# Performance work log

Hardware: AMD Instinct MI355X
Metric: run time of the kernel (lower is better)

Reference implementation:

```python
import jax, jax.numpy as jnp
import numpy as np

EMBED_DIM = 1024
N_HEADS = 16
HEAD_DIM = EMBED_DIM // N_HEADS


def setup_inputs() -> dict:
    key = jax.random.key(0)
    k_x, k_qw, k_qb, k_ow, k_ob = jax.random.split(key, 5)
    s = 1.0 / np.sqrt(EMBED_DIM)
    return {
        "x": jax.random.normal(k_x, (2, 2048, EMBED_DIM), dtype=jnp.float32),
        "qkv_w": jax.random.uniform(k_qw, (3 * EMBED_DIM, EMBED_DIM), jnp.float32, -s, s),
        "qkv_b": jax.random.uniform(k_qb, (3 * EMBED_DIM,), jnp.float32, -s, s),
        "out_w": jax.random.uniform(k_ow, (EMBED_DIM, EMBED_DIM), jnp.float32, -s, s),
        "out_b": jax.random.uniform(k_ob, (EMBED_DIM,), jnp.float32, -s, s),
    }


def reference(x, qkv_w, qkv_b, out_w, out_b):
    B, S, E = x.shape
    # fused QKV projection (torch Linear: x @ W^T + b)
    qkv = x @ qkv_w.T + qkv_b                      # [B,S,3E]
    qkv = qkv.reshape(B, S, N_HEADS, 3 * HEAD_DIM).transpose(0, 2, 1, 3)  # [B,H,S,3d]
    q, k, v = jnp.split(qkv, 3, axis=-1)           # each [B,H,S,d]
    scores = jnp.einsum("bhqd,bhkd->bhqk", q, k) / jnp.sqrt(jnp.float32(HEAD_DIM))
    weights = jax.nn.softmax(scores, axis=-1)      # [B,H,S,S]
    attn = jnp.einsum("bhqk,bhkd->bhqd", weights, v)
    attn = attn.transpose(0, 2, 1, 3).reshape(B, S, E)
    return attn @ out_w.T + out_b
```

## Files before the change

### kernel.cpp

```cpp
#include <hip/hip_runtime.h>
#include <hip/hip_bf16.h>


#define E_DIM   1024
#define NHEADS  16
#define HDIM    64
#define SEQ     2048
#define TOK     4096
#define QKV_DIM 3072
#define QK_STRIDE 2048
#define QSCALE_F 0.18033688011112042f

typedef __attribute__((ext_vector_type(8))) short bf16x8;
typedef __attribute__((ext_vector_type(4))) float f32x4;
typedef __attribute__((ext_vector_type(4))) int   i32x4;
typedef __attribute__((ext_vector_type(2))) int   i32x2;
typedef __attribute__((ext_vector_type(2))) __bf16 bf16x2_t;

#if __has_builtin(__builtin_amdgcn_exp2f)
#define EXP2F(x) __builtin_amdgcn_exp2f(x)
#else
#define EXP2F(x) exp2f(x)
#endif

__device__ __forceinline__ unsigned pack2bf(float a, float b) {
#if __has_builtin(__builtin_amdgcn_cvt_pk_bf16_f32)
    union { bf16x2_t v; unsigned u; } u;
    u.v = __builtin_amdgcn_cvt_pk_bf16_f32(a, b);
    return u.u;
#else
    union { float f; unsigned u; } ua, ub; ua.f = a; ub.f = b;
    unsigned ra = ua.u + 0x7FFF + ((ua.u >> 16) & 1);
    unsigned rb = ub.u + 0x7FFF + ((ub.u >> 16) & 1);
    return (ra >> 16) | (rb & 0xFFFF0000u);
#endif
}

__device__ __forceinline__ unsigned short f2bf(float x) {
    return (unsigned short)(pack2bf(x, x) & 0xFFFFu);
}

__device__ __forceinline__ void load_lds16(const void* g, void* l) {
    __builtin_amdgcn_global_load_lds(
        (const __attribute__((address_space(1))) void*)g,
        (__attribute__((address_space(3))) void*)l, 16, 0, 0);
}

__device__ __forceinline__ bf16x8 lds_read8(const unsigned short* p) {
    union { i32x4 i; bf16x8 b; } u;
    u.i = *(const i32x4*)p;
    return u.b;
}

__device__ __forceinline__ f32x4 mfma16(bf16x8 a, bf16x8 b, f32x4 c) {
    return __builtin_amdgcn_mfma_f32_16x16x32_bf16(a, b, c, 0, 0, 0);
}

__global__ void cast3_kernel(const float* __restrict__ a, unsigned short* __restrict__ oa, int na4,
                             const float* __restrict__ b, unsigned short* __restrict__ ob, int nb4,
                             const float* __restrict__ c, unsigned short* __restrict__ oc) {
    int i = blockIdx.x * blockDim.x + threadIdx.x;
    const float* src; unsigned short* dst; int j;
    if (i < na4)            { src = a; dst = oa; j = i; }
    else if (i < na4 + nb4) { src = b; dst = ob; j = i - na4; }
    else                    { src = c; dst = oc; j = i - na4 - nb4; }
    f32x4 v = ((const f32x4*)src)[j];
    union { i32x2 i2; unsigned u[2]; } o;
    o.u[0] = pack2bf(v.x, v.y);
    o.u[1] = pack2bf(v.z, v.w);
    ((i32x2*)dst)[j] = o.i2;
}

__global__ __launch_bounds__(256, 3)
void gemm_qkv_kernel(const unsigned short* __restrict__ A,
                     const unsigned short* __restrict__ B,
                     const float* __restrict__ bias,
                     unsigned short* __restrict__ qk,
                     unsigned short* __restrict__ vT,
                     int K) {
    __shared__ __align__(16) unsigned short As[128 * 64];
    __shared__ __align__(16) unsigned short Bs[128 * 64];

    const int tid  = threadIdx.x;
    const int wave = tid >> 6, lane = tid & 63;
    const int quad = lane >> 4, l16 = lane & 15;
    const int flat = blockIdx.y * 24 + blockIdx.x;
    const int xcd = flat & 7, idx = flat >> 3;
    const int row_blk = (xcd >> 1) * 8 + idx / 12;
    const int col_blk = (xcd & 1) * 12 + idx % 12;
    const int row0 = row_blk * 128, col0 = col_blk * 128;
    const int wr = (wave >> 1) * 64, wc = (wave & 1) * 64;

    f32x4 acc[4][4];
#pragma unroll
    for (int i = 0; i < 4; ++i)
#pragma unroll
        for (int j = 0; j < 4; ++j) acc[i][j] = (f32x4){0.f, 0.f, 0.f, 0.f};

    const int nkt = K >> 6;
    for (int kt = 0; kt < nkt; ++kt) {
        const int k0 = kt << 6;
#pragma unroll
        for (int i = 0; i < 4; ++i) {
            int p = i * 256 + tid;
            int r = p >> 3;
            int kc = (p & 7) ^ (r & 7);
            load_lds16(A + (size_t)(row0 + r) * K + k0 + kc * 8, &As[p * 8]);
        }
#pragma unroll
        for (int i = 0; i < 4; ++i) {
            int p = i * 256 + tid;
            int r = p >> 3;
            int kc = (p & 7) ^ (r & 7);
            load_lds16(B + (size_t)(col0 + r) * K + k0 + kc * 8, &Bs[p * 8]);
        }
        __syncthreads();

#pragma unroll
        for (int ks = 0; ks < 2; ++ks) {
            bf16x8 af[4], bfr[4];
#pragma unroll
            for (int rb = 0; rb < 4; ++rb) {
                int r_l  = wr + rb * 16 + l16;
                int phys = (ks * 4 + quad) ^ (l16 & 7);
                af[rb] = lds_read8(&As[r_l * 64 + phys * 8]);
            }
#pragma unroll
            for (int cb = 0; cb < 4; ++cb) {
                int r_l  = wc + cb * 16 + l16;
                int phys = (ks * 4 + quad) ^ (l16 & 7);
                bfr[cb] = lds_read8(&Bs[r_l * 64 + phys * 8]);
            }
#pragma unroll
            for (int rb = 0; rb < 4; ++rb)
#pragma unroll
                for (int cb = 0; cb < 4; ++cb)
                    acc[rb][cb] = mfma16(af[rb], bfr[cb], acc[rb][cb]);
        }
        __syncthreads();
    }

#pragma unroll
    for (int rb = 0; rb < 4; ++rb)
#pragma unroll
        for (int cb = 0; cb < 4; ++cb) {
            int col = col0 + wc + cb * 16 + l16;
            int h    = col / 192;
            int part = col - h * 192;
            float bv = bias[col];
            int row_b = row0 + wr + rb * 16 + quad * 4;
            float v[4];
#pragma unroll
            for (int reg = 0; reg < 4; ++reg) v[reg] = acc[rb][cb][reg] + bv;
            if (part < 128) {
                float sc = (part < 64) ? QSCALE_F : 1.0f;
                size_t base = (size_t)h * 128 + part;
#pragma unroll
                for (int reg = 0; reg < 4; ++reg)
                    qk[(size_t)(row_b + reg) * QK_STRIDE + base] = f2bf(v[reg] * sc);
            } else {
                int i  = part - 128;
                int b  = row_b >> 11;
                int s  = row_b & 2047;
                i32x2 pk;
                pk.x = (int)pack2bf(v[0], v[1]);
                pk.y = (int)pack2bf(v[2], v[3]);
                *(i32x2*)&vT[(((size_t)(b * 16 + h)) * 64 + i) * SEQ + s] = pk;
            }
        }
}

__global__ __launch_bounds__(256, 2)
void gemm2_kernel(const unsigned short* __restrict__ A,
                  const unsigned short* __restrict__ B,
                  const float* __restrict__ bias,
                  float* __restrict__ C, int M, int N, int K) {
    __shared__ __align__(16) unsigned short As[128 * 64];
    __shared__ __align__(16) unsigned short Bs[64 * 64];

    const int tid  = threadIdx.x;
    const int wave = tid >> 6, lane = tid & 63;
    const int quad = lane >> 4, l16 = lane & 15;
    const int flat = blockIdx.y * 16 + blockIdx.x;
    const int xcd = flat & 7, idx = flat >> 3;
    const int row_blk = (xcd >> 1) * 8 + (idx >> 3);
    const int col_blk = (xcd & 1) * 8 + (idx & 7);
    const int row0 = row_blk * 128, col0 = col_blk * 64;
    const int wr = wave * 32;

    f32x4 acc[2][4];
#pragma unroll
    for (int i = 0; i < 2; ++i)
#pragma unroll
        for (int j = 0; j < 4; ++j) acc[i][j] = (f32x4){0.f, 0.f, 0.f, 0.f};

    const int nkt = K >> 6;
    for (int kt = 0; kt < nkt; ++kt) {
        const int k0 = kt << 6;
#pragma unroll
        for (int i = 0; i < 4; ++i) {
            int p = i * 256 + tid;
            int r = p >> 3;
            int kc = (p & 7) ^ (r & 7);
            load_lds16(A + (size_t)(row0 + r) * K + k0 + kc * 8, &As[p * 8]);
        }
#pragma unroll
        for (int i = 0; i < 2; ++i) {
            int p = i * 256 + tid;
            int r = p >> 3;
            int kc = (p & 7) ^ (r & 7);
            load_lds16(B + (size_t)(col0 + r) * K + k0 + kc * 8, &Bs[p * 8]);
        }
        __syncthreads();

#pragma unroll
        for (int ks = 0; ks < 2; ++ks) {
            bf16x8 af[2], bfr[4];
#pragma unroll
            for (int rb = 0; rb < 2; ++rb) {
                int r_l  = wr + rb * 16 + l16;
                int phys = (ks * 4 + quad) ^ (l16 & 7);
                af[rb] = lds_read8(&As[r_l * 64 + phys * 8]);
            }
#pragma unroll
            for (int cb = 0; cb < 4; ++cb) {
                int r_l  = cb * 16 + l16;
                int phys = (ks * 4 + quad) ^ (l16 & 7);
                bfr[cb] = lds_read8(&Bs[r_l * 64 + phys * 8]);
            }
#pragma unroll
            for (int rb = 0; rb < 2; ++rb)
#pragma unroll
                for (int cb = 0; cb < 4; ++cb)
                    acc[rb][cb] = mfma16(af[rb], bfr[cb], acc[rb][cb]);
        }
        __syncthreads();
    }

#pragma unroll
    for (int rb = 0; rb < 2; ++rb)
#pragma unroll
        for (int cb = 0; cb < 4; ++cb) {
            int col = col0 + cb * 16 + l16;
            float bv = bias[col];
#pragma unroll
            for (int reg = 0; reg < 4; ++reg) {
                int row = row0 + wr + rb * 16 + quad * 4 + reg;
                C[(size_t)row * N + col] = acc[rb][cb][reg] + bv;
            }
        }
}

__global__ __launch_bounds__(512, 4)
void attn_kernel(const unsigned short* __restrict__ qk,
                 const unsigned short* __restrict__ vT,
                 unsigned short* __restrict__ attn) {
    __shared__ __align__(16) unsigned short Ks[128 * 64];
    __shared__ __align__(16) unsigned short Vs[64 * 128];
    __shared__ __align__(16) unsigned short Ps[8][16 * 128];

    const int tid  = threadIdx.x;
    const int wave = tid >> 6, lane = tid & 63;
    const int quad = lane >> 4, l16 = lane & 15;

    const int flat = blockIdx.y * 16 + blockIdx.x;
    const int swz  = (flat & 7) * 64 + (flat >> 3);
    const int bh = swz >> 4;
    const int b = bh >> 4, h = bh & 15;
    const int q0 = (swz & 15) * 128;
    const size_t rowbase = (size_t)b * SEQ;
    const int qtok = q0 + wave * 16 + l16;

    const int sw3 = l16 & 7;
    const unsigned short* Kb0 = &Ks[l16 * 64 + ((quad ^ sw3) * 8)];
    const unsigned short* Kb1 = &Ks[l16 * 64 + (((4 + quad) ^ sw3) * 8)];
    const unsigned short* Vb[4] = {
        &Vs[l16 * 128 + (((0 * 4 + quad) ^ l16) * 8)],
        &Vs[l16 * 128 + (((1 * 4 + quad) ^ l16) * 8)],
        &Vs[l16 * 128 + (((2 * 4 + quad) ^ l16) * 8)],
        &Vs[l16 * 128 + (((3 * 4 + quad) ^ l16) * 8)] };
    unsigned short* Pw[8];
#pragma unroll
    for (int cb = 0; cb < 8; ++cb)
        Pw[cb] = &Ps[wave][l16 * 128 + (((cb * 2 + (quad >> 1)) ^ sw3) * 8) + (quad & 1) * 4];
    const unsigned short* Pr[4];
#pragma unroll
    for (int ks2 = 0; ks2 < 4; ++ks2)
        Pr[ks2] = &Ps[wave][l16 * 128 + (((ks2 * 4 + quad) ^ sw3) * 8)];

    const unsigned short* kg[2]; unsigned short* lk[2];
    const unsigned short* vg[2]; unsigned short* lv[2];
#pragma unroll
    for (int i = 0; i < 2; ++i) {
        int p = i * 512 + tid;
        { int r = p >> 3; int kc = (p & 7) ^ (r & 7);
          kg[i] = qk + (rowbase) * QK_STRIDE + h * 128 + 64 + (size_t)r * QK_STRIDE + kc * 8;
          lk[i] = &Ks[p * 8]; }
        { int r = p >> 4; int c = (p & 15) ^ (r & 15);
          vg[i] = vT + (size_t)bh * 64 * SEQ + (size_t)r * SEQ + c * 8;
          lv[i] = &Vs[p * 8]; }
    }

    bf16x8 qf[2];
#pragma unroll
    for (int ks = 0; ks < 2; ++ks) {
        const unsigned short* p =
            qk + (rowbase + qtok) * QK_STRIDE + h * 128 + ks * 32 + quad * 8;
        union { i32x4 i; bf16x8 b; } u;
        u.i = *(const i32x4*)p;
        qf[ks] = u.b;
    }

    f32x4 o[4];
#pragma unroll
    for (int ib = 0; ib < 4; ++ib) o[ib] = (f32x4){0.f, 0.f, 0.f, 0.f};
    float l_s = 0.f;

    for (int kt = 0; kt < SEQ / 128; ++kt) {
#pragma unroll
        for (int i = 0; i < 2; ++i) {
            load_lds16(kg[i], lk[i]);
            load_lds16(vg[i], lv[i]);
            kg[i] += 128 * QK_STRIDE;
            vg[i] += 128;
        }
        __syncthreads();

        f32x4 s[8];
#pragma unroll
        for (int cb = 0; cb < 8; ++cb) s[cb] = (f32x4){0.f, 0.f, 0.f, 0.f};
        __builtin_amdgcn_s_setprio(1);
#pragma unroll
        for (int cb = 0; cb < 8; ++cb) {
            bf16x8 kf0 = lds_read8(Kb0 + cb * 1024);
            s[cb] = mfma16(kf0, qf[0], s[cb]);
        }
#pragma unroll
        for (int cb = 0; cb < 8; ++cb) {
            bf16x8 kf1 = lds_read8(Kb1 + cb * 1024);
            s[cb] = mfma16(kf1, qf[1], s[cb]);
        }
        __builtin_amdgcn_s_setprio(0);

#pragma unroll
        for (int cb = 0; cb < 8; ++cb)
#pragma unroll
            for (int r = 0; r < 4; ++r) s[cb][r] = EXP2F(s[cb][r]);
        {
            f32x4 t0 = s[0] + s[1], t1 = s[2] + s[3];
            f32x4 t2 = s[4] + s[5], t3 = s[6] + s[7];
            t0 += t1; t2 += t3; t0 += t2;
            float rs = (t0[0] + t0[1]) + (t0[2] + t0[3]);
            rs += __shfl_xor(rs, 16);
            rs += __shfl_xor(rs, 32);
            l_s += rs;
        }

#pragma unroll
        for (int cb = 0; cb < 8; ++cb) {
            i32x2 pk;
            pk.x = (int)pack2bf(s[cb][0], s[cb][1]);
            pk.y = (int)pack2bf(s[cb][2], s[cb][3]);
            *(i32x2*)Pw[cb] = pk;
        }
        __asm__ volatile("s_waitcnt lgkmcnt(0)" ::: "memory");
        __builtin_amdgcn_s_setprio(1);
#pragma unroll
        for (int ks2 = 0; ks2 < 4; ++ks2) {
            bf16x8 pf = lds_read8(Pr[ks2]);
#pragma unroll
            for (int ib = 0; ib < 4; ++ib) {
                bf16x8 vf = lds_read8(Vb[ks2] + ib * 2048);
                o[ib] = mfma16(pf, vf, o[ib]);
            }
        }
        __builtin_amdgcn_s_setprio(0);
        __syncthreads();
    }

    float il[4];
#pragma unroll
    for (int r = 0; r < 4; ++r) il[r] = 1.0f / __shfl(l_s, quad * 4 + r);
#pragma unroll
    for (int ib = 0; ib < 4; ++ib)
#pragma unroll
        for (int r = 0; r < 4; ++r) {
            int t = q0 + wave * 16 + quad * 4 + r;
            attn[(rowbase + t) * E_DIM + h * 64 + ib * 16 + l16] =
                f2bf(o[ib][r] * il[r]);
        }
}

extern "C" void kernel_launch(void* const* d_in, const int* in_sizes, int n_in,
                              void* d_out, int out_size, void* d_ws, size_t ws_size,
                              hipStream_t stream) {
    const float* x     = (const float*)d_in[0];
    const float* qkv_w = (const float*)d_in[1];
    const float* qkv_b = (const float*)d_in[2];
    const float* out_w = (const float*)d_in[3];
    const float* out_b = (const float*)d_in[4];

    char* ws = (char*)d_ws;
    unsigned short* xb   = (unsigned short*)(ws);
    unsigned short* wqkv = (unsigned short*)(ws + 8388608);
    unsigned short* wout = (unsigned short*)(ws + 14680064);
    unsigned short* qk   = (unsigned short*)(ws + 16777216);
    unsigned short* attn = (unsigned short*)(ws + 33554432);
    unsigned short* vT   = (unsigned short*)(ws + 41943040);

    cast3_kernel<<<8192, 256, 0, stream>>>(x, xb, 1048576,
                                           qkv_w, wqkv, 786432,
                                           out_w, wout);

    gemm_qkv_kernel<<<dim3(24, 32), 256, 0, stream>>>(
        xb, wqkv, qkv_b, qk, vT, E_DIM);

    attn_kernel<<<dim3(16, 32), 512, 0, stream>>>(qk, vT, attn);

    gemm2_kernel<<<dim3(16, 32), 256, 0, stream>>>(
        attn, wout, out_b, (float*)d_out, TOK, E_DIM, E_DIM);
}
```

Measured before the change: 185.7 us.

## Keep softmax probabilities in registers by permuting V layout to match MFMA fragments

The attention kernel no longer stages the probability tile through per-wave LDS. P fragments for the PV MFMA are packed directly from the QK^T accumulator registers. To keep the math consistent, the QKV GEMM epilogue writes V^T with a permuted sequence index so the key ordering matches the register fragment layout. This removes LDS writes, a wait and LDS reads per tile, and frees shared memory that may help occupancy. The cost is a more complex index permutation in the V store.

```diff
diff --git a/kernel.cpp b/kernel.cpp
--- a/kernel.cpp
+++ b/kernel.cpp
@@ -161,11 +161,14 @@
             } else {
                 int i  = part - 128;
                 int b  = row_b >> 11;
-                int s  = row_b & 2047;
+                int s0 = row_b & 2047;
+                int kk = s0 & 127;
+                int cc = kk >> 4, qq = (kk >> 2) & 3;
+                int sp = (s0 & ~127) | ((cc >> 1) << 5) | (qq << 3) | ((cc & 1) << 2);
                 i32x2 pk;
                 pk.x = (int)pack2bf(v[0], v[1]);
                 pk.y = (int)pack2bf(v[2], v[3]);
-                *(i32x2*)&vT[(((size_t)(b * 16 + h)) * 64 + i) * SEQ + s] = pk;
+                *(i32x2*)&vT[(((size_t)(b * 16 + h)) * 64 + i) * SEQ + sp] = pk;
             }
         }
 }
@@ -257,7 +260,6 @@
                  unsigned short* __restrict__ attn) {
     __shared__ __align__(16) unsigned short Ks[128 * 64];
     __shared__ __align__(16) unsigned short Vs[64 * 128];
-    __shared__ __align__(16) unsigned short Ps[8][16 * 128];
 
     const int tid  = threadIdx.x;
     const int wave = tid >> 6, lane = tid & 63;
@@ -279,14 +281,6 @@
         &Vs[l16 * 128 + (((1 * 4 + quad) ^ l16) * 8)],
         &Vs[l16 * 128 + (((2 * 4 + quad) ^ l16) * 8)],
         &Vs[l16 * 128 + (((3 * 4 + quad) ^ l16) * 8)] };
-    unsigned short* Pw[8];
-#pragma unroll
-    for (int cb = 0; cb < 8; ++cb)
-        Pw[cb] = &Ps[wave][l16 * 128 + (((cb * 2 + (quad >> 1)) ^ sw3) * 8) + (quad & 1) * 4];
-    const unsigned short* Pr[4];
-#pragma unroll
-    for (int ks2 = 0; ks2 < 4; ++ks2)
-        Pr[ks2] = &Ps[wave][l16 * 128 + (((ks2 * 4 + quad) ^ sw3) * 8)];
 
     const unsigned short* kg[2]; unsigned short* lk[2];
     const unsigned short* vg[2]; unsigned short* lv[2];
@@ -356,18 +350,15 @@
             l_s += rs;
         }
 
-#pragma unroll
-        for (int cb = 0; cb < 8; ++cb) {
-            i32x2 pk;
-            pk.x = (int)pack2bf(s[cb][0], s[cb][1]);
-            pk.y = (int)pack2bf(s[cb][2], s[cb][3]);
-            *(i32x2*)Pw[cb] = pk;
-        }
-        __asm__ volatile("s_waitcnt lgkmcnt(0)" ::: "memory");
         __builtin_amdgcn_s_setprio(1);
 #pragma unroll
         for (int ks2 = 0; ks2 < 4; ++ks2) {
-            bf16x8 pf = lds_read8(Pr[ks2]);
+            union { i32x4 i; bf16x8 b; } pu;
+            pu.i.x = (int)pack2bf(s[2 * ks2][0], s[2 * ks2][1]);
+            pu.i.y = (int)pack2bf(s[2 * ks2][2], s[2 * ks2][3]);
+            pu.i.z = (int)pack2bf(s[2 * ks2 + 1][0], s[2 * ks2 + 1][1]);
+            pu.i.w = (int)pack2bf(s[2 * ks2 + 1][2], s[2 * ks2 + 1][3]);
+            bf16x8 pf = pu.b;
 #pragma unroll
             for (int ib = 0; ib < 4; ++ib) {
                 bf16x8 vf = lds_read8(Vb[ks2] + ib * 2048);
```

New measurement: 179.6 us. 1.03x faster.
